# Kernel tuning notes

Measured on AMD Instinct MI355X. Metric: run time of the kernel, lower is better.

Reference implementation:

```python
import jax, jax.numpy as jnp
import numpy as np

NUM_HEADS = 12

def rel_indices(N):
    # [N, N, 3] = (dx, dy, dist^2) between patches on an img x img grid
    img = int(N ** 0.5)
    ind = jnp.arange(img)[None, :] - jnp.arange(img)[:, None]      # [img, img]
    indx = jnp.tile(ind, (img, img))                               # [N, N]
    indy = jnp.repeat(jnp.repeat(ind, img, axis=0), img, axis=1)   # [N, N]
    indd = indx ** 2 + indy ** 2
    return jnp.stack([indx, indy, indd], axis=-1).astype(jnp.float32)

def setup_inputs() -> dict:
    key = jax.random.key(0)
    ks = jax.random.split(key, 8)
    B, N, C, H = 16, 576, 768, NUM_HEADS
    std = 0.02  # trunc_normal init scale in the original
    return {
        "x": jax.random.normal(ks[0], (B, N, C), jnp.float32),
        "w_qk": jax.random.normal(ks[1], (C, 2 * C), jnp.float32) * std,
        "w_v": jax.random.normal(ks[2], (C, C), jnp.float32) * std,
        "w_proj": jax.random.normal(ks[3], (C, C), jnp.float32) * std,
        "b_proj": jnp.zeros((C,), jnp.float32),
        "w_pos": jax.random.normal(ks[4], (3, H), jnp.float32) * std,
        "b_pos": jnp.zeros((H,), jnp.float32),
        "gating": jnp.ones((H,), jnp.float32),
    }

def reference(x, w_qk, w_v, w_proj, b_proj, w_pos, b_pos, gating):
    B, N, C = x.shape
    H = NUM_HEADS
    Dh = C // H
    scale = Dh ** -0.5

    # q, k: [B, H, N, Dh]
    qk = (x @ w_qk).reshape(B, N, 2, H, Dh)
    q = jnp.transpose(qk[:, :, 0], (0, 2, 1, 3))
    k = jnp.transpose(qk[:, :, 1], (0, 2, 1, 3))

    # content scores, softmax over keys
    patch_score = jax.nn.softmax(
        jnp.einsum("bhnd,bhmd->bhnm", q, k) * scale, axis=-1)

    # positional scores: rel_indices [N,N,3] -> [H,N,N], softmax over keys
    rel = rel_indices(N)
    pos_logits = jnp.einsum("nmk,kh->hnm", rel, w_pos) + b_pos[:, None, None]
    pos_score = jax.nn.softmax(pos_logits, axis=-1)  # [H, N, N]

    # sigmoid gating + renormalization
    g = jax.nn.sigmoid(gating)[None, :, None, None]
    attn = (1.0 - g) * patch_score + g * pos_score[None]
    attn = attn / jnp.sum(attn, axis=-1, keepdims=True)

    # v: [B, H, N, Dh]
    v = jnp.transpose((x @ w_v).reshape(B, N, H, Dh), (0, 2, 1, 3))

    out = jnp.einsum("bhnm,bhmd->bnhd", attn, v).reshape(B, N, C)
    out = out @ w_proj + b_proj
    return (out, attn, v)
```

## Files before the change

### kernel.cpp

```cpp
#include <hip/hip_runtime.h>
#include <hip/hip_bf16.h>

typedef __bf16 bf16;
typedef __attribute__((ext_vector_type(4))) __bf16 bf16x4;
typedef __attribute__((ext_vector_type(8))) __bf16 bf16x8;
typedef __attribute__((ext_vector_type(4))) float floatx4;

#define BB 16
#define NN 576
#define CC 768
#define HH 12
#define DH 64

#define GLOAD_LDS16(gp, lp) __builtin_amdgcn_global_load_lds( \
    (const __attribute__((address_space(1))) unsigned int*)(const void*)(gp), \
    (__attribute__((address_space(3))) unsigned int*)(void*)(lp), 16, 0, 0)

__global__ void k_convert(const float* __restrict__ in, bf16* __restrict__ out, int n4){
  int i = blockIdx.x*blockDim.x + threadIdx.x;
  if (i < n4){
    float4 f = ((const float4*)in)[i];
    bf16x4 o;
    o[0]=(bf16)f.x; o[1]=(bf16)f.y; o[2]=(bf16)f.z; o[3]=(bf16)f.w;
    ((bf16x4*)out)[i] = o;
  }
}

__global__ void k_transpose(const float* __restrict__ src, bf16* __restrict__ dst, int R, int Cc){
  __shared__ float tile[32][33];
  int c0 = blockIdx.x*32, r0 = blockIdx.y*32;
  int tx = threadIdx.x & 31, ty = threadIdx.x >> 5;
  #pragma unroll
  for (int i=0;i<4;i++)
    tile[ty + i*8][tx] = src[(size_t)(r0 + ty + i*8)*Cc + c0 + tx];
  __syncthreads();
  #pragma unroll
  for (int i=0;i<4;i++)
    dst[(size_t)(c0 + ty + i*8)*R + r0 + tx] = (bf16)tile[tx][ty + i*8];
}

__global__ __launch_bounds__(256) void k_pos(const float* __restrict__ w_pos, float* __restrict__ pos){
  int t = threadIdx.x, wv = t>>6, lane = t&63;
  int rowid = blockIdx.x*4 + wv;
  int h = rowid / NN, n = rowid % NN;
  float w0 = w_pos[h], w1 = w_pos[HH + h], w2 = w_pos[2*HH + h];
  int nx = n % 24, ny = n / 24;
  float e[9]; float mx = -1e30f;
  #pragma unroll
  for (int j=0;j<9;j++){
    int m = lane + 64*j;
    float dx = (float)(m % 24 - nx);
    float dy = (float)(m / 24 - ny);
    float l = dx*w0 + dy*w1 + (dx*dx + dy*dy)*w2;
    e[j] = l; mx = fmaxf(mx, l);
  }
  #pragma unroll
  for (int s=1;s<64;s<<=1) mx = fmaxf(mx, __shfl_xor(mx, s, 64));
  float sum = 0.f;
  #pragma unroll
  for (int j=0;j<9;j++){ e[j] = __expf(e[j]-mx); sum += e[j]; }
  #pragma unroll
  for (int s=1;s<64;s<<=1) sum += __shfl_xor(sum, s, 64);
  float inv = 1.f/sum;
  float* dst = pos + (size_t)rowid*NN;
  #pragma unroll
  for (int j=0;j<9;j++) dst[lane + 64*j] = e[j]*inv;
}

__device__ __forceinline__ void gemm128_main(
    const bf16* __restrict__ A, const bf16* __restrict__ B,
    int lda, int ldb, int K, bf16* As, bf16* Bs, floatx4 (*acc)[4])
{
  int t = threadIdx.x;
  int w = t>>6, m16 = t&15, q = (t&63)>>4;
  int wr = (w>>1)*64, wc = (w&1)*64;
  int sr = t>>2, kg = (t&3)*8;
  bf16* ldsA = As + w*512;
  bf16* ldsB = Bs + w*512;
  for (int k0 = 0; k0 < K; k0 += 32){
    GLOAD_LDS16(A + (size_t)sr*lda      + k0 + kg, ldsA);
    GLOAD_LDS16(A + (size_t)(sr+64)*lda + k0 + kg, ldsA + 2048);
    GLOAD_LDS16(B + (size_t)sr*ldb      + k0 + kg, ldsB);
    GLOAD_LDS16(B + (size_t)(sr+64)*ldb + k0 + kg, ldsB + 2048);
    __syncthreads();
    bf16x8 af[4], bfv[4];
    #pragma unroll
    for (int rt=0;rt<4;rt++) af[rt]  = *(const bf16x8*)&As[(wr + rt*16 + m16)*32 + q*8];
    #pragma unroll
    for (int ct=0;ct<4;ct++) bfv[ct] = *(const bf16x8*)&Bs[(wc + ct*16 + m16)*32 + q*8];
    #pragma unroll
    for (int rt=0;rt<4;rt++)
      #pragma unroll
      for (int ct=0;ct<4;ct++)
        acc[rt][ct] = __builtin_amdgcn_mfma_f32_16x16x32_bf16(af[rt], bfv[ct], acc[rt][ct], 0, 0, 0);
    __syncthreads();
  }
}

__global__ __launch_bounds__(256) void k_gemm1(
    const bf16* __restrict__ x_bf, const bf16* __restrict__ wcatT,
    bf16* __restrict__ q_bf, bf16* __restrict__ k_bf,
    bf16* __restrict__ vt_bf, float* __restrict__ v_out)
{
  __shared__ bf16 As[128*32];
  __shared__ bf16 Bs[128*32];
  int cb = blockIdx.x % 18, rb = blockIdx.x / 18;
  int rowBase = rb*128, colBase = cb*128;
  floatx4 zero = {0.f,0.f,0.f,0.f};
  floatx4 acc[4][4];
  #pragma unroll
  for (int a=0;a<4;a++)
    #pragma unroll
    for (int b=0;b<4;b++) acc[a][b] = zero;
  gemm128_main(x_bf + (size_t)rowBase*CC, wcatT + (size_t)colBase*CC, CC, CC, CC, As, Bs, acc);
  int t = threadIdx.x;
  int w = t>>6, m16 = t&15, q = (t&63)>>4;
  int wr = (w>>1)*64, wc = (w&1)*64;
  #pragma unroll
  for (int rt=0;rt<4;rt++){
    #pragma unroll
    for (int i=0;i<4;i++){
      int row = rowBase + wr + rt*16 + q*4 + i;
      int b = row / NN, n = row % NN;
      #pragma unroll
      for (int ct=0;ct<4;ct++){
        int col = colBase + wc + ct*16 + m16;
        float val = acc[rt][ct][i];
        if (col < 2*CC){
          int s = col / CC, rem = col % CC;
          int h = rem >> 6, d = rem & 63;
          bf16* dst = s ? k_bf : q_bf;
          dst[(((size_t)(b*HH + h)*NN + n) << 6) + d] = (bf16)val;
        } else {
          int rem = col - 2*CC;
          int h = rem >> 6, d = rem & 63;
          v_out[(((size_t)(b*HH + h)*NN + n) << 6) + d] = val;
          vt_bf[((size_t)(b*HH + h)*DH + d)*NN + n] = (bf16)val;
        }
      }
    }
  }
}

__global__ __launch_bounds__(256) void k_attn_pv(
    const bf16* __restrict__ q_bf, const bf16* __restrict__ k_bf,
    const bf16* __restrict__ vt_bf,
    const float* __restrict__ pos, const float* __restrict__ gating,
    float* __restrict__ attn_out, bf16* __restrict__ out1_bf)
{
  __shared__ bf16 Qs[16][72];
  __shared__ bf16 Ks[64][72];
  __shared__ float S[16][592];
  int qt = blockIdx.x % 36, bh = blockIdx.x / 36;
  int b = bh / HH, h = bh % HH;
  int n0 = qt*16;
  int t = threadIdx.x;
  int wv = t>>6, m16 = t&15, q = (t&63)>>4;
  const bf16* Qg = q_bf + ((size_t)bh*NN + n0)*DH;
  const bf16* Kg = k_bf + (size_t)bh*NN*DH;
  { int r = t >> 4, c4 = (t & 15)*4;
    *(bf16x4*)&Qs[r][c4] = *(const bf16x4*)&Qg[r*DH + c4]; }
  for (int kt=0; kt<9; kt++){
    __syncthreads();
    { int r = t>>2, cg = (t&3)*16;
      *(bf16x8*)&Ks[r][cg]   = *(const bf16x8*)&Kg[(kt*64 + r)*DH + cg];
      *(bf16x8*)&Ks[r][cg+8] = *(const bf16x8*)&Kg[(kt*64 + r)*DH + cg + 8]; }
    __syncthreads();
    floatx4 acc = {0.f,0.f,0.f,0.f};
    #pragma unroll
    for (int ks=0; ks<2; ks++){
      bf16x8 afr = *(const bf16x8*)&Qs[m16][ks*32 + q*8];
      bf16x8 bfr = *(const bf16x8*)&Ks[wv*16 + m16][ks*32 + q*8];
      acc = __builtin_amdgcn_mfma_f32_16x16x32_bf16(afr, bfr, acc, 0, 0, 0);
    }
    #pragma unroll
    for (int i=0;i<4;i++)
      S[q*4 + i][kt*64 + wv*16 + m16] = acc[i] * 0.125f;
  }
  __syncthreads();
  int row = t >> 4, sub = t & 15;
  int n = n0 + row;
  float vals[36];
  float mx = -1e30f;
  #pragma unroll
  for (int j=0;j<36;j++){ float xv = S[row][sub + 16*j]; vals[j]=xv; mx = fmaxf(mx,xv); }
  #pragma unroll
  for (int s=1;s<16;s<<=1) mx = fmaxf(mx, __shfl_xor(mx, s, 64));
  float ps = 0.f;
  #pragma unroll
  for (int j=0;j<36;j++){ vals[j] = __expf(vals[j]-mx); ps += vals[j]; }
  #pragma unroll
  for (int s=1;s<16;s<<=1) ps += __shfl_xor(ps, s, 64);
  float g = 1.f/(1.f + __expf(-gating[h]));
  float ig = (1.f - g)/ps;
  const float* posrow = pos + ((size_t)h*NN + n)*NN;
  float bs = 0.f;
  #pragma unroll
  for (int j=0;j<36;j++){ float a = ig*vals[j] + g*posrow[sub + 16*j]; vals[j]=a; bs += a; }
  #pragma unroll
  for (int s=1;s<16;s<<=1) bs += __shfl_xor(bs, s, 64);
  float inv = 1.f/bs;
  __syncthreads();
  float* arow = attn_out + ((size_t)bh*NN + n)*NN;
  char* prow = (char*)(&S[0][0]) + row*2368 + ((row&3)<<4);
  #pragma unroll
  for (int j=0;j<36;j++){
    float a = vals[j]*inv;
    arow[sub + 16*j] = a;
    *(bf16*)(prow + 2*(sub + 16*j)) = (bf16)a;
  }
  __syncthreads();
  floatx4 pacc = {0.f,0.f,0.f,0.f};
  const bf16* vrow = vt_bf + ((size_t)bh*DH + wv*16 + m16)*NN;
  const char* pbase = (const char*)(&S[0][0]) + m16*2368 + ((m16&3)<<4) + q*16;
  #pragma unroll
  for (int c=0;c<18;c++){
    bf16x8 afr = *(const bf16x8*)(pbase + c*64);
    bf16x8 bfr = *(const bf16x8*)&vrow[c*32 + q*8];
    pacc = __builtin_amdgcn_mfma_f32_16x16x32_bf16(afr, bfr, pacc, 0, 0, 0);
  }
  bf16* obase = out1_bf + ((size_t)(b*NN + n0))*CC + h*DH + wv*16 + m16;
  #pragma unroll
  for (int i=0;i<4;i++)
    obase[(size_t)(q*4 + i)*CC] = (bf16)pacc[i];
}

__global__ __launch_bounds__(256) void k_proj(
    const bf16* __restrict__ out1_bf, const bf16* __restrict__ wprojT,
    const float* __restrict__ b_proj, float* __restrict__ out)
{
  __shared__ bf16 As[128*32];
  __shared__ bf16 Bs[128*32];
  int cb = blockIdx.x % 6, rb = blockIdx.x / 6;
  int rowBase = rb*128, colBase = cb*128;
  floatx4 zero = {0.f,0.f,0.f,0.f};
  floatx4 acc[4][4];
  #pragma unroll
  for (int a=0;a<4;a++)
    #pragma unroll
    for (int b=0;b<4;b++) acc[a][b] = zero;
  gemm128_main(out1_bf + (size_t)rowBase*CC, wprojT + (size_t)colBase*CC, CC, CC, CC, As, Bs, acc);
  int t = threadIdx.x;
  int w = t>>6, m16 = t&15, q = (t&63)>>4;
  int wr = (w>>1)*64, wc = (w&1)*64;
  #pragma unroll
  for (int rt=0;rt<4;rt++){
    #pragma unroll
    for (int i=0;i<4;i++){
      int row = rowBase + wr + rt*16 + q*4 + i;
      #pragma unroll
      for (int ct=0;ct<4;ct++){
        int col = colBase + wc + ct*16 + m16;
        out[(size_t)row*CC + col] = acc[rt][ct][i] + b_proj[col];
      }
    }
  }
}

extern "C" void kernel_launch(void* const* d_in, const int* in_sizes, int n_in,
                              void* d_out, int out_size, void* d_ws, size_t ws_size,
                              hipStream_t stream)
{
  (void)in_sizes; (void)n_in; (void)out_size; (void)ws_size;
  const float* x      = (const float*)d_in[0];
  const float* w_qk   = (const float*)d_in[1];
  const float* w_v    = (const float*)d_in[2];
  const float* w_proj = (const float*)d_in[3];
  const float* b_proj = (const float*)d_in[4];
  const float* w_pos  = (const float*)d_in[5];
  const float* gating = (const float*)d_in[7];

  float* out_ptr  = (float*)d_out;
  float* attn_ptr = out_ptr + (size_t)BB*NN*CC;
  float* v_ptr    = attn_ptr + (size_t)BB*HH*NN*NN;

  char* w = (char*)d_ws;
  bf16* x_bf    = (bf16*)(w);
  bf16* wcatT   = (bf16*)(w + 14155776);
  bf16* wprojT  = (bf16*)(w + 17694720);
  bf16* q_bf    = (bf16*)(w + 18874368);
  bf16* k_bf    = (bf16*)(w + 33030144);
  bf16* vt_bf   = (bf16*)(w + 47185920);
  float* pos    = (float*)(w + 61341696);
  bf16* out1_bf = x_bf;

  k_convert<<<6912, 256, 0, stream>>>(x, x_bf, (BB*NN*CC)/4);
  k_transpose<<<dim3(48,24), 256, 0, stream>>>(w_qk, wcatT, CC, 2*CC);
  k_transpose<<<dim3(24,24), 256, 0, stream>>>(w_v, wcatT + (size_t)2*CC*CC, CC, CC);
  k_transpose<<<dim3(24,24), 256, 0, stream>>>(w_proj, wprojT, CC, CC);
  k_pos<<<(HH*NN)/4, 256, 0, stream>>>(w_pos, pos);
  k_gemm1<<<72*18, 256, 0, stream>>>(x_bf, wcatT, q_bf, k_bf, vt_bf, v_ptr);
  k_attn_pv<<<192*36, 256, 0, stream>>>(q_bf, k_bf, vt_bf, pos, gating, attn_ptr, out1_bf);
  k_proj<<<72*6, 256, 0, stream>>>(out1_bf, wprojT, b_proj, out_ptr);
}
```

Before: 557.9 us.

## Restructure attention kernel to 64-query tiles with register-resident scores

The attention kernel now processes 64 query rows per block (4 waves of 16) instead of 16. Scores stay in MFMA accumulator registers, so the fp32 LDS score buffer and its round-trip are gone. K tiles are loaded with direct global-to-LDS loads and an XOR swizzle, and the 1/sqrt(d) scale is folded into Q at the projection epilogue. The positional softmax table is stored in bf16 to halve its traffic, which costs precision in pos_score. The kernel now uses 144 accumulator VGPRs and a 75KB LDS tile, which may limit occupancy.

```diff
diff --git a/kernel.cpp b/kernel.cpp
--- a/kernel.cpp
+++ b/kernel.cpp
@@ -39,7 +39,7 @@
     dst[(size_t)(c0 + ty + i*8)*R + r0 + tx] = (bf16)tile[tx][ty + i*8];
 }
 
-__global__ __launch_bounds__(256) void k_pos(const float* __restrict__ w_pos, float* __restrict__ pos){
+__global__ __launch_bounds__(256) void k_pos(const float* __restrict__ w_pos, bf16* __restrict__ pos){
   int t = threadIdx.x, wv = t>>6, lane = t&63;
   int rowid = blockIdx.x*4 + wv;
   int h = rowid / NN, n = rowid % NN;
@@ -62,9 +62,9 @@
   #pragma unroll
   for (int s=1;s<64;s<<=1) sum += __shfl_xor(sum, s, 64);
   float inv = 1.f/sum;
-  float* dst = pos + (size_t)rowid*NN;
-  #pragma unroll
-  for (int j=0;j<9;j++) dst[lane + 64*j] = e[j]*inv;
+  bf16* dst = pos + (size_t)rowid*NN;
+  #pragma unroll
+  for (int j=0;j<9;j++) dst[lane + 64*j] = (bf16)(e[j]*inv);
 }
 
 __device__ __forceinline__ void gemm128_main(
@@ -130,7 +130,8 @@
           int s = col / CC, rem = col % CC;
           int h = rem >> 6, d = rem & 63;
           bf16* dst = s ? k_bf : q_bf;
-          dst[(((size_t)(b*HH + h)*NN + n) << 6) + d] = (bf16)val;
+          float sv = s ? val : val*0.125f;
+          dst[(((size_t)(b*HH + h)*NN + n) << 6) + d] = (bf16)sv;
         } else {
           int rem = col - 2*CC;
           int h = rem >> 6, d = rem & 63;
@@ -142,87 +143,125 @@
   }
 }
 
-__global__ __launch_bounds__(256) void k_attn_pv(
+__global__ __launch_bounds__(256, 2) void k_attn_pv(
     const bf16* __restrict__ q_bf, const bf16* __restrict__ k_bf,
     const bf16* __restrict__ vt_bf,
-    const float* __restrict__ pos, const float* __restrict__ gating,
+    const bf16* __restrict__ pos, const float* __restrict__ gating,
     float* __restrict__ attn_out, bf16* __restrict__ out1_bf)
 {
-  __shared__ bf16 Qs[16][72];
-  __shared__ bf16 Ks[64][72];
-  __shared__ float S[16][592];
-  int qt = blockIdx.x % 36, bh = blockIdx.x / 36;
+  __shared__ __align__(16) char smem[64*1200];
+  int qt = blockIdx.x % 9, bh = blockIdx.x / 9;
   int b = bh / HH, h = bh % HH;
-  int n0 = qt*16;
+  int n0 = qt*64;
   int t = threadIdx.x;
   int wv = t>>6, m16 = t&15, q = (t&63)>>4;
-  const bf16* Qg = q_bf + ((size_t)bh*NN + n0)*DH;
+
+  const bf16* qrow = q_bf + ((size_t)bh*NN + n0 + wv*16 + m16)*DH;
+  bf16x8 afr0 = *(const bf16x8*)&qrow[q*8];
+  bf16x8 afr1 = *(const bf16x8*)&qrow[32 + q*8];
+
   const bf16* Kg = k_bf + (size_t)bh*NN*DH;
-  { int r = t >> 4, c4 = (t & 15)*4;
-    *(bf16x4*)&Qs[r][c4] = *(const bf16x4*)&Qg[r*DH + c4]; }
+  floatx4 acc[36];
+  #pragma unroll
+  for (int T=0;T<36;T++) acc[T] = (floatx4){0.f,0.f,0.f,0.f};
+
+  int key0 = t>>3, g16 = (t&7) ^ (key0 & 7);
+  #pragma unroll
   for (int kt=0; kt<9; kt++){
     __syncthreads();
-    { int r = t>>2, cg = (t&3)*16;
-      *(bf16x8*)&Ks[r][cg]   = *(const bf16x8*)&Kg[(kt*64 + r)*DH + cg];
-      *(bf16x8*)&Ks[r][cg+8] = *(const bf16x8*)&Kg[(kt*64 + r)*DH + cg + 8]; }
+    const bf16* src0 = Kg + (size_t)(kt*64 + key0)*DH + g16*8;
+    GLOAD_LDS16(src0,           smem + wv*1024);
+    GLOAD_LDS16(src0 + 32*DH,   smem + 4096 + wv*1024);
     __syncthreads();
-    floatx4 acc = {0.f,0.f,0.f,0.f};
-    #pragma unroll
-    for (int ks=0; ks<2; ks++){
-      bf16x8 afr = *(const bf16x8*)&Qs[m16][ks*32 + q*8];
-      bf16x8 bfr = *(const bf16x8*)&Ks[wv*16 + m16][ks*32 + q*8];
-      acc = __builtin_amdgcn_mfma_f32_16x16x32_bf16(afr, bfr, acc, 0, 0, 0);
-    }
-    #pragma unroll
-    for (int i=0;i<4;i++)
-      S[q*4 + i][kt*64 + wv*16 + m16] = acc[i] * 0.125f;
-  }
+    #pragma unroll
+    for (int ct=0; ct<4; ct++){
+      int key = ct*16 + m16;
+      int swz = key & 7;
+      bf16x8 b0 = *(const bf16x8*)(smem + key*128 + ((q ^ swz)<<4));
+      bf16x8 b1 = *(const bf16x8*)(smem + key*128 + (((4 + q) ^ swz)<<4));
+      acc[kt*4+ct] = __builtin_amdgcn_mfma_f32_16x16x32_bf16(afr0, b0, acc[kt*4+ct], 0, 0, 0);
+      acc[kt*4+ct] = __builtin_amdgcn_mfma_f32_16x16x32_bf16(afr1, b1, acc[kt*4+ct], 0, 0, 0);
+    }
+  }
+
+  float mx[4], ps[4], bs[4];
+  #pragma unroll
+  for (int i=0;i<4;i++) mx[i] = -1e30f;
+  #pragma unroll
+  for (int T=0;T<36;T++)
+    #pragma unroll
+    for (int i=0;i<4;i++) mx[i] = fmaxf(mx[i], acc[T][i]);
+  #pragma unroll
+  for (int s=1;s<16;s<<=1)
+    #pragma unroll
+    for (int i=0;i<4;i++) mx[i] = fmaxf(mx[i], __shfl_xor(mx[i], s, 64));
+  #pragma unroll
+  for (int i=0;i<4;i++) ps[i] = 0.f;
+  #pragma unroll
+  for (int T=0;T<36;T++)
+    #pragma unroll
+    for (int i=0;i<4;i++){ float e = __expf(acc[T][i]-mx[i]); acc[T][i]=e; ps[i]+=e; }
+  #pragma unroll
+  for (int s=1;s<16;s<<=1)
+    #pragma unroll
+    for (int i=0;i<4;i++) ps[i] += __shfl_xor(ps[i], s, 64);
+
+  float g = 1.f/(1.f + __expf(-gating[h]));
+  float ig[4];
+  #pragma unroll
+  for (int i=0;i<4;i++){ ig[i] = (1.f-g)/ps[i]; bs[i] = 0.f; }
+
+  int rowq = n0 + wv*16 + q*4;
+  const bf16* posb = pos + ((size_t)h*NN + rowq)*NN + m16;
+  #pragma unroll
+  for (int T=0;T<36;T++)
+    #pragma unroll
+    for (int i=0;i<4;i++){
+      float p = (float)posb[(size_t)i*NN + T*16];
+      float a = ig[i]*acc[T][i] + g*p;
+      acc[T][i] = a; bs[i] += a;
+    }
+  #pragma unroll
+  for (int s=1;s<16;s<<=1)
+    #pragma unroll
+    for (int i=0;i<4;i++) bs[i] += __shfl_xor(bs[i], s, 64);
+  float inv[4];
+  #pragma unroll
+  for (int i=0;i<4;i++) inv[i] = 1.f/bs[i];
+
   __syncthreads();
-  int row = t >> 4, sub = t & 15;
-  int n = n0 + row;
-  float vals[36];
-  float mx = -1e30f;
-  #pragma unroll
-  for (int j=0;j<36;j++){ float xv = S[row][sub + 16*j]; vals[j]=xv; mx = fmaxf(mx,xv); }
-  #pragma unroll
-  for (int s=1;s<16;s<<=1) mx = fmaxf(mx, __shfl_xor(mx, s, 64));
-  float ps = 0.f;
-  #pragma unroll
-  for (int j=0;j<36;j++){ vals[j] = __expf(vals[j]-mx); ps += vals[j]; }
-  #pragma unroll
-  for (int s=1;s<16;s<<=1) ps += __shfl_xor(ps, s, 64);
-  float g = 1.f/(1.f + __expf(-gating[h]));
-  float ig = (1.f - g)/ps;
-  const float* posrow = pos + ((size_t)h*NN + n)*NN;
-  float bs = 0.f;
-  #pragma unroll
-  for (int j=0;j<36;j++){ float a = ig*vals[j] + g*posrow[sub + 16*j]; vals[j]=a; bs += a; }
-  #pragma unroll
-  for (int s=1;s<16;s<<=1) bs += __shfl_xor(bs, s, 64);
-  float inv = 1.f/bs;
+  float* arow = attn_out + ((size_t)bh*NN + rowq)*NN + m16;
+  char* prow = smem + (size_t)(wv*16 + q*4)*1200 + m16*2;
+  #pragma unroll
+  for (int T=0;T<36;T++)
+    #pragma unroll
+    for (int i=0;i<4;i++){
+      float a = acc[T][i]*inv[i];
+      arow[(size_t)i*NN + T*16] = a;
+      *(bf16*)(prow + i*1200 + T*32) = (bf16)a;
+    }
   __syncthreads();
-  float* arow = attn_out + ((size_t)bh*NN + n)*NN;
-  char* prow = (char*)(&S[0][0]) + row*2368 + ((row&3)<<4);
-  #pragma unroll
-  for (int j=0;j<36;j++){
-    float a = vals[j]*inv;
-    arow[sub + 16*j] = a;
-    *(bf16*)(prow + 2*(sub + 16*j)) = (bf16)a;
-  }
-  __syncthreads();
-  floatx4 pacc = {0.f,0.f,0.f,0.f};
-  const bf16* vrow = vt_bf + ((size_t)bh*DH + wv*16 + m16)*NN;
-  const char* pbase = (const char*)(&S[0][0]) + m16*2368 + ((m16&3)<<4) + q*16;
+
+  floatx4 pacc[4];
+  #pragma unroll
+  for (int ct=0;ct<4;ct++) pacc[ct] = (floatx4){0.f,0.f,0.f,0.f};
+  const char* pbase = smem + (size_t)(wv*16 + m16)*1200 + q*16;
+  const bf16* vbase = vt_bf + (size_t)bh*DH*NN + q*8;
   #pragma unroll
   for (int c=0;c<18;c++){
     bf16x8 afr = *(const bf16x8*)(pbase + c*64);
-    bf16x8 bfr = *(const bf16x8*)&vrow[c*32 + q*8];
-    pacc = __builtin_amdgcn_mfma_f32_16x16x32_bf16(afr, bfr, pacc, 0, 0, 0);
-  }
-  bf16* obase = out1_bf + ((size_t)(b*NN + n0))*CC + h*DH + wv*16 + m16;
-  #pragma unroll
-  for (int i=0;i<4;i++)
-    obase[(size_t)(q*4 + i)*CC] = (bf16)pacc[i];
+    #pragma unroll
+    for (int ct=0;ct<4;ct++){
+      bf16x8 bfr = *(const bf16x8*)&vbase[(size_t)(ct*16+m16)*NN + c*32];
+      pacc[ct] = __builtin_amdgcn_mfma_f32_16x16x32_bf16(afr, bfr, pacc[ct], 0, 0, 0);
+    }
+  }
+  bf16* obase = out1_bf + ((size_t)(b*NN + rowq))*CC + h*DH + m16;
+  #pragma unroll
+  for (int ct=0;ct<4;ct++)
+    #pragma unroll
+    for (int i=0;i<4;i++)
+      obase[(size_t)i*CC + ct*16] = (bf16)pacc[ct][i];
 }
 
 __global__ __launch_bounds__(256) void k_proj(
@@ -281,15 +320,15 @@
   bf16* q_bf    = (bf16*)(w + 18874368);
   bf16* k_bf    = (bf16*)(w + 33030144);
   bf16* vt_bf   = (bf16*)(w + 47185920);
-  float* pos    = (float*)(w + 61341696);
+  bf16* pos_bf  = (bf16*)(w + 61341696);
   bf16* out1_bf = x_bf;
 
   k_convert<<<6912, 256, 0, stream>>>(x, x_bf, (BB*NN*CC)/4);
   k_transpose<<<dim3(48,24), 256, 0, stream>>>(w_qk, wcatT, CC, 2*CC);
   k_transpose<<<dim3(24,24), 256, 0, stream>>>(w_v, wcatT + (size_t)2*CC*CC, CC, CC);
   k_transpose<<<dim3(24,24), 256, 0, stream>>>(w_proj, wprojT, CC, CC);
-  k_pos<<<(HH*NN)/4, 256, 0, stream>>>(w_pos, pos);
+  k_pos<<<(HH*NN)/4, 256, 0, stream>>>(w_pos, pos_bf);
   k_gemm1<<<72*18, 256, 0, stream>>>(x_bf, wcatT, q_bf, k_bf, vt_bf, v_ptr);
-  k_attn_pv<<<192*36, 256, 0, stream>>>(q_bf, k_bf, vt_bf, pos, gating, attn_ptr, out1_bf);
+  k_attn_pv<<<192*9, 256, 0, stream>>>(q_bf, k_bf, vt_bf, pos_bf, gating, attn_ptr, out1_bf);
   k_proj<<<72*6, 256, 0, stream>>>(out1_bf, wprojT, b_proj, out_ptr);
 }
```

New measurement: 541.2 us. 3.0% less time.
